# Kernel tuning notes

Measured on AMD Instinct MI355X. Metric: run time of the kernel, lower is better.

## Reference

```python
import jax, jax.numpy as jnp
import numpy as np

N, T = 64, 256
TOTAL_NODES, C_IN = 25, 128          # c = 3200
NUM_SEEDS, C_OUT = 5, 3              # seeds flat dim = 15
NEW_NODES = 20
LIN_IN = TOTAL_NODES * C_IN + NUM_SEEDS * C_OUT  # 3215


def setup_inputs() -> dict:
    key = jax.random.key(0)
    k1, k2, k3 = jax.random.split(key, 3)
    x = jax.random.normal(k1, (N, T, TOTAL_NODES * C_IN), dtype=jnp.float32)
    seeds = jax.random.normal(k2, (N, T, NUM_SEEDS, C_OUT), dtype=jnp.float32)
    # Stacked weights of the `new_nodes` cloned Linear(LIN_IN, C_OUT) layers.
    W = jax.random.normal(k3, (NEW_NODES, C_OUT, LIN_IN), dtype=jnp.float32) * 0.02
    b = jnp.zeros((NEW_NODES, C_OUT), dtype=jnp.float32)
    return {"x": x, "seeds": seeds, "W": W, "b": b}


def reference(x, seeds, W, b):
    n, t, _ = x.shape
    mix = jnp.concatenate([x, seeds.reshape(n, t, -1)], axis=2)  # [n,t,LIN_IN]
    # Fuse all cloned small Linears into one batched GEMM, then layout as
    # torch.stack([...], dim=3): output [n, t, c_out, new_nodes].
    out = jnp.einsum('ntc,koc->ntok', mix, W) + b.T  # b.T: [c_out, new_nodes]
    return out
```

## Files before the change

kernel.cpp:

```cpp
#include <hip/hip_runtime.h>


#define NROWS    16384
#define CIN      3200
#define SEED_K   15
#define LIN_IN   3215
#define NCOL     60
#define KB_MAIN  100
#define KB_TOT   101
#define WB_ELEMS (KB_TOT * 4 * 64 * 8)
#define PART_N   (NROWS * NCOL)

typedef __attribute__((ext_vector_type(8))) __bf16 bf16x8;
typedef __attribute__((ext_vector_type(4))) float f32x4;
typedef __attribute__((ext_vector_type(8))) unsigned short ushort8;

__device__ unsigned short Wb_g[WB_ELEMS];
__device__ __align__(16) float bias_g[64];

__device__ inline unsigned short f2bf_rne(float f) {
    unsigned int u = __builtin_bit_cast(unsigned int, f);
    u += 0x7fffu + ((u >> 16) & 1u);
    return (unsigned short)(u >> 16);
}

__device__ inline bf16x8 to_bf16x8(f32x4 a0, f32x4 a1) {
    ushort8 u;
    u[0] = f2bf_rne(a0[0]); u[1] = f2bf_rne(a0[1]);
    u[2] = f2bf_rne(a0[2]); u[3] = f2bf_rne(a0[3]);
    u[4] = f2bf_rne(a1[0]); u[5] = f2bf_rne(a1[1]);
    u[6] = f2bf_rne(a1[2]); u[7] = f2bf_rne(a1[3]);
    return __builtin_bit_cast(bf16x8, u);
}

__global__ void prep_B(const float* __restrict__ W, const float* __restrict__ b) {
    int idx = blockIdx.x * blockDim.x + threadIdx.x;
    if (idx >= WB_ELEMS) return;
    if (idx < 64) bias_g[idx] = (idx < NCOL) ? b[(idx % 20) * 3 + (idx / 20)] : 0.f;
    int jj   = idx & 7;
    int lane = (idx >> 3) & 63;
    int nt   = (idx >> 9) & 3;
    int kb   = idx >> 11;
    int k = kb * 32 + (lane >> 4) * 8 + jj;
    int n = nt * 16 + (lane & 15);
    float v = 0.0f;
    if (k < LIN_IN && n < NCOL) {
        int o = n / 20, kn = n % 20;
        v = W[(kn * 3 + o) * LIN_IN + k];
    }
    Wb_g[idx] = f2bf_rne(v);
}

__global__ __launch_bounds__(256, 6) void gen_nodes_part(
    const float* __restrict__ x, const float* __restrict__ seeds,
    float* __restrict__ part) {
    const int lane = threadIdx.x & 63;
    const int wave = threadIdx.x >> 6;
    const int quad = lane >> 4;
    const int l15  = lane & 15;
    const int rg   = blockIdx.x >> 1;
    const int kh   = blockIdx.x & 1;
    const int row_base = rg * 16;
    const int arow = row_base + l15;

    const float* xrow = x + (size_t)arow * CIN + quad * 8;

    f32x4 acc[4];
#pragma unroll
    for (int i = 0; i < 4; ++i) acc[i] = (f32x4){0.f, 0.f, 0.f, 0.f};

    const int kend = kh * 50 + 50;
    int kb = kh * 50 + wave;
    const f32x4* ap = (const f32x4*)(xrow + kb * 32);
    f32x4 a0 = __builtin_nontemporal_load(ap);
    f32x4 a1 = __builtin_nontemporal_load(ap + 1);

#pragma unroll 2
    while (kb < kend) {
        int kn = kb + 4;
        int kc = (kn < KB_MAIN - 1) ? kn : (KB_MAIN - 1);
        const f32x4* apn = (const f32x4*)(xrow + kc * 32);
        f32x4 p0 = __builtin_nontemporal_load(apn);
        f32x4 p1 = __builtin_nontemporal_load(apn + 1);

        const unsigned short* bb = Wb_g + (size_t)kb * 2048 + lane * 8;
        bf16x8 b0 = *(const bf16x8*)(bb);
        bf16x8 b1 = *(const bf16x8*)(bb + 512);
        bf16x8 b2 = *(const bf16x8*)(bb + 1024);
        bf16x8 b3 = *(const bf16x8*)(bb + 1536);
        bf16x8 af = to_bf16x8(a0, a1);
        acc[0] = __builtin_amdgcn_mfma_f32_16x16x32_bf16(af, b0, acc[0], 0, 0, 0);
        acc[1] = __builtin_amdgcn_mfma_f32_16x16x32_bf16(af, b1, acc[1], 0, 0, 0);
        acc[2] = __builtin_amdgcn_mfma_f32_16x16x32_bf16(af, b2, acc[2], 0, 0, 0);
        acc[3] = __builtin_amdgcn_mfma_f32_16x16x32_bf16(af, b3, acc[3], 0, 0, 0);

        a0 = p0; a1 = p1; kb = kn;
    }

    if (kh == 1 && wave == 3) {
        const float* srow = seeds + (size_t)arow * SEED_K;
        f32x4 s0 = {0.f, 0.f, 0.f, 0.f}, s1 = {0.f, 0.f, 0.f, 0.f};
#pragma unroll
        for (int j = 0; j < 4; ++j) {
            int c = quad * 8 + j;
            if (c < SEED_K) s0[j] = srow[c];
            if (c + 4 < SEED_K) s1[j] = srow[c + 4];
        }
        bf16x8 af = to_bf16x8(s0, s1);
        const unsigned short* bb = Wb_g + (size_t)KB_MAIN * 2048 + lane * 8;
        bf16x8 b0 = *(const bf16x8*)(bb);
        bf16x8 b1 = *(const bf16x8*)(bb + 512);
        bf16x8 b2 = *(const bf16x8*)(bb + 1024);
        bf16x8 b3 = *(const bf16x8*)(bb + 1536);
        acc[0] = __builtin_amdgcn_mfma_f32_16x16x32_bf16(af, b0, acc[0], 0, 0, 0);
        acc[1] = __builtin_amdgcn_mfma_f32_16x16x32_bf16(af, b1, acc[1], 0, 0, 0);
        acc[2] = __builtin_amdgcn_mfma_f32_16x16x32_bf16(af, b2, acc[2], 0, 0, 0);
        acc[3] = __builtin_amdgcn_mfma_f32_16x16x32_bf16(af, b3, acc[3], 0, 0, 0);
    }

    __shared__ float red[3][16][68];
    if (wave != 0) {
#pragma unroll
        for (int nt = 0; nt < 4; ++nt)
#pragma unroll
            for (int r = 0; r < 4; ++r)
                red[wave - 1][quad * 4 + r][nt * 16 + l15] = acc[nt][r];
    }
    __syncthreads();

    if (wave == 0) {
        float* pdst = part + (size_t)kh * PART_N;
#pragma unroll
        for (int nt = 0; nt < 4; ++nt) {
            int j = nt * 16 + l15;
            if (j < NCOL) {
#pragma unroll
                for (int r = 0; r < 4; ++r) {
                    int m = quad * 4 + r;
                    float v = acc[nt][r] + red[0][m][j] + red[1][m][j] + red[2][m][j];
                    pdst[(size_t)(row_base + m) * NCOL + j] = v;
                }
            }
        }
    }
}

__global__ __launch_bounds__(256) void combine(
    const float* __restrict__ part, float* __restrict__ out) {
    int idx = blockIdx.x * 256 + threadIdx.x;
    int fl  = idx * 4;
    f32x4 p0 = *(const f32x4*)(part + fl);
    f32x4 p1 = *(const f32x4*)(part + PART_N + fl);
    int jb = fl % NCOL;
    f32x4 bv = *(const f32x4*)(bias_g + jb);
    f32x4 o = p0 + p1 + bv;
    *(f32x4*)(out + fl) = o;
}

extern "C" void kernel_launch(void* const* d_in, const int* in_sizes, int n_in,
                              void* d_out, int out_size, void* d_ws, size_t ws_size,
                              hipStream_t stream) {
    const float* x     = (const float*)d_in[0];
    const float* seeds = (const float*)d_in[1];
    const float* W     = (const float*)d_in[2];
    const float* b     = (const float*)d_in[3];
    float* out  = (float*)d_out;
    float* part = (float*)d_ws;

    prep_B<<<(WB_ELEMS + 255) / 256, 256, 0, stream>>>(W, b);
    gen_nodes_part<<<2048, 256, 0, stream>>>(x, seeds, part);
    combine<<<PART_N / 4 / 256, 256, 0, stream>>>(part, out);
}
```

Baseline: 310.6 us.

## Process two 16-row tiles per block to reuse each B fragment load

Each block now handles 32 rows instead of 16, issuing two A-tile loads per k-step and reusing the same four bf16 B fragments for eight MFMAs. The grid is halved, occupancy hint lowered to 4, and the shared reduction buffer doubled. This is meant to halve the weight reloads per row and give more memory-level parallelism per wave, at the cost of more registers and fewer resident blocks.

```diff
diff --git a/kernel.cpp b/kernel.cpp
--- a/kernel.cpp
+++ b/kernel.cpp
@@ -51,7 +51,7 @@
     Wb_g[idx] = f2bf_rne(v);
 }
 
-__global__ __launch_bounds__(256, 6) void gen_nodes_part(
+__global__ __launch_bounds__(256, 4) void gen_nodes_part(
     const float* __restrict__ x, const float* __restrict__ seeds,
     float* __restrict__ part) {
     const int lane = threadIdx.x & 63;
@@ -60,85 +60,109 @@
     const int l15  = lane & 15;
     const int rg   = blockIdx.x >> 1;
     const int kh   = blockIdx.x & 1;
-    const int row_base = rg * 16;
+    const int row_base = rg * 32;
     const int arow = row_base + l15;
 
-    const float* xrow = x + (size_t)arow * CIN + quad * 8;
+    const float* xrow0 = x + (size_t)arow * CIN + quad * 8;
+    const float* xrow1 = xrow0 + (size_t)16 * CIN;
 
-    f32x4 acc[4];
+    f32x4 acc[2][4];
 #pragma unroll
-    for (int i = 0; i < 4; ++i) acc[i] = (f32x4){0.f, 0.f, 0.f, 0.f};
+    for (int t = 0; t < 2; ++t)
+#pragma unroll
+        for (int i = 0; i < 4; ++i) acc[t][i] = (f32x4){0.f, 0.f, 0.f, 0.f};
 
     const int kend = kh * 50 + 50;
     int kb = kh * 50 + wave;
-    const f32x4* ap = (const f32x4*)(xrow + kb * 32);
-    f32x4 a0 = __builtin_nontemporal_load(ap);
-    f32x4 a1 = __builtin_nontemporal_load(ap + 1);
+    {
+        const f32x4* ap0 = (const f32x4*)(xrow0 + kb * 32);
+        const f32x4* ap1 = (const f32x4*)(xrow1 + kb * 32);
+        f32x4 a0 = __builtin_nontemporal_load(ap0);
+        f32x4 a1 = __builtin_nontemporal_load(ap0 + 1);
+        f32x4 a2 = __builtin_nontemporal_load(ap1);
+        f32x4 a3 = __builtin_nontemporal_load(ap1 + 1);
 
 #pragma unroll 2
-    while (kb < kend) {
-        int kn = kb + 4;
-        int kc = (kn < KB_MAIN - 1) ? kn : (KB_MAIN - 1);
-        const f32x4* apn = (const f32x4*)(xrow + kc * 32);
-        f32x4 p0 = __builtin_nontemporal_load(apn);
-        f32x4 p1 = __builtin_nontemporal_load(apn + 1);
+        while (kb < kend) {
+            int kn = kb + 4;
+            int kc = (kn < KB_MAIN - 1) ? kn : (KB_MAIN - 1);
+            const f32x4* apn0 = (const f32x4*)(xrow0 + kc * 32);
+            const f32x4* apn1 = (const f32x4*)(xrow1 + kc * 32);
+            f32x4 p0 = __builtin_nontemporal_load(apn0);
+            f32x4 p1 = __builtin_nontemporal_load(apn0 + 1);
+            f32x4 p2 = __builtin_nontemporal_load(apn1);
+            f32x4 p3 = __builtin_nontemporal_load(apn1 + 1);
 
-        const unsigned short* bb = Wb_g + (size_t)kb * 2048 + lane * 8;
-        bf16x8 b0 = *(const bf16x8*)(bb);
-        bf16x8 b1 = *(const bf16x8*)(bb + 512);
-        bf16x8 b2 = *(const bf16x8*)(bb + 1024);
-        bf16x8 b3 = *(const bf16x8*)(bb + 1536);
-        bf16x8 af = to_bf16x8(a0, a1);
-        acc[0] = __builtin_amdgcn_mfma_f32_16x16x32_bf16(af, b0, acc[0], 0, 0, 0);
-        acc[1] = __builtin_amdgcn_mfma_f32_16x16x32_bf16(af, b1, acc[1], 0, 0, 0);
-        acc[2] = __builtin_amdgcn_mfma_f32_16x16x32_bf16(af, b2, acc[2], 0, 0, 0);
-        acc[3] = __builtin_amdgcn_mfma_f32_16x16x32_bf16(af, b3, acc[3], 0, 0, 0);
+            const unsigned short* bb = Wb_g + (size_t)kb * 2048 + lane * 8;
+            bf16x8 b0 = *(const bf16x8*)(bb);
+            bf16x8 b1 = *(const bf16x8*)(bb + 512);
+            bf16x8 b2 = *(const bf16x8*)(bb + 1024);
+            bf16x8 b3 = *(const bf16x8*)(bb + 1536);
+            bf16x8 af0 = to_bf16x8(a0, a1);
+            bf16x8 af1 = to_bf16x8(a2, a3);
+            acc[0][0] = __builtin_amdgcn_mfma_f32_16x16x32_bf16(af0, b0, acc[0][0], 0, 0, 0);
+            acc[0][1] = __builtin_amdgcn_mfma_f32_16x16x32_bf16(af0, b1, acc[0][1], 0, 0, 0);
+            acc[0][2] = __builtin_amdgcn_mfma_f32_16x16x32_bf16(af0, b2, acc[0][2], 0, 0, 0);
+            acc[0][3] = __builtin_amdgcn_mfma_f32_16x16x32_bf16(af0, b3, acc[0][3], 0, 0, 0);
+            acc[1][0] = __builtin_amdgcn_mfma_f32_16x16x32_bf16(af1, b0, acc[1][0], 0, 0, 0);
+            acc[1][1] = __builtin_amdgcn_mfma_f32_16x16x32_bf16(af1, b1, acc[1][1], 0, 0, 0);
+            acc[1][2] = __builtin_amdgcn_mfma_f32_16x16x32_bf16(af1, b2, acc[1][2], 0, 0, 0);
+            acc[1][3] = __builtin_amdgcn_mfma_f32_16x16x32_bf16(af1, b3, acc[1][3], 0, 0, 0);
 
-        a0 = p0; a1 = p1; kb = kn;
+            a0 = p0; a1 = p1; a2 = p2; a3 = p3; kb = kn;
+        }
     }
 
     if (kh == 1 && wave == 3) {
-        const float* srow = seeds + (size_t)arow * SEED_K;
-        f32x4 s0 = {0.f, 0.f, 0.f, 0.f}, s1 = {0.f, 0.f, 0.f, 0.f};
-#pragma unroll
-        for (int j = 0; j < 4; ++j) {
-            int c = quad * 8 + j;
-            if (c < SEED_K) s0[j] = srow[c];
-            if (c + 4 < SEED_K) s1[j] = srow[c + 4];
-        }
-        bf16x8 af = to_bf16x8(s0, s1);
         const unsigned short* bb = Wb_g + (size_t)KB_MAIN * 2048 + lane * 8;
         bf16x8 b0 = *(const bf16x8*)(bb);
         bf16x8 b1 = *(const bf16x8*)(bb + 512);
         bf16x8 b2 = *(const bf16x8*)(bb + 1024);
         bf16x8 b3 = *(const bf16x8*)(bb + 1536);
-        acc[0] = __builtin_amdgcn_mfma_f32_16x16x32_bf16(af, b0, acc[0], 0, 0, 0);
-        acc[1] = __builtin_amdgcn_mfma_f32_16x16x32_bf16(af, b1, acc[1], 0, 0, 0);
-        acc[2] = __builtin_amdgcn_mfma_f32_16x16x32_bf16(af, b2, acc[2], 0, 0, 0);
-        acc[3] = __builtin_amdgcn_mfma_f32_16x16x32_bf16(af, b3, acc[3], 0, 0, 0);
+#pragma unroll
+        for (int t = 0; t < 2; ++t) {
+            const float* srow = seeds + (size_t)(arow + t * 16) * SEED_K;
+            f32x4 s0 = {0.f, 0.f, 0.f, 0.f}, s1 = {0.f, 0.f, 0.f, 0.f};
+#pragma unroll
+            for (int j = 0; j < 4; ++j) {
+                int c = quad * 8 + j;
+                if (c < SEED_K) s0[j] = srow[c];
+                if (c + 4 < SEED_K) s1[j] = srow[c + 4];
+            }
+            bf16x8 af = to_bf16x8(s0, s1);
+            acc[t][0] = __builtin_amdgcn_mfma_f32_16x16x32_bf16(af, b0, acc[t][0], 0, 0, 0);
+            acc[t][1] = __builtin_amdgcn_mfma_f32_16x16x32_bf16(af, b1, acc[t][1], 0, 0, 0);
+            acc[t][2] = __builtin_amdgcn_mfma_f32_16x16x32_bf16(af, b2, acc[t][2], 0, 0, 0);
+            acc[t][3] = __builtin_amdgcn_mfma_f32_16x16x32_bf16(af, b3, acc[t][3], 0, 0, 0);
+        }
     }
 
-    __shared__ float red[3][16][68];
+    __shared__ float red[3][32][68];
     if (wave != 0) {
 #pragma unroll
-        for (int nt = 0; nt < 4; ++nt)
+        for (int t = 0; t < 2; ++t)
 #pragma unroll
-            for (int r = 0; r < 4; ++r)
-                red[wave - 1][quad * 4 + r][nt * 16 + l15] = acc[nt][r];
+            for (int nt = 0; nt < 4; ++nt)
+#pragma unroll
+                for (int r = 0; r < 4; ++r)
+                    red[wave - 1][t * 16 + quad * 4 + r][nt * 16 + l15] = acc[t][nt][r];
     }
     __syncthreads();
 
     if (wave == 0) {
         float* pdst = part + (size_t)kh * PART_N;
 #pragma unroll
-        for (int nt = 0; nt < 4; ++nt) {
-            int j = nt * 16 + l15;
-            if (j < NCOL) {
+        for (int t = 0; t < 2; ++t) {
 #pragma unroll
-                for (int r = 0; r < 4; ++r) {
-                    int m = quad * 4 + r;
-                    float v = acc[nt][r] + red[0][m][j] + red[1][m][j] + red[2][m][j];
-                    pdst[(size_t)(row_base + m) * NCOL + j] = v;
+            for (int nt = 0; nt < 4; ++nt) {
+                int j = nt * 16 + l15;
+                if (j < NCOL) {
+#pragma unroll
+                    for (int r = 0; r < 4; ++r) {
+                        int m = t * 16 + quad * 4 + r;
+                        float v = acc[t][nt][r] + red[0][m][j] + red[1][m][j] + red[2][m][j];
+                        pdst[(size_t)(row_base + m) * NCOL + j] = v;
+                    }
                 }
             }
         }
@@ -168,6 +192,6 @@
     float* part = (float*)d_ws;
 
     prep_B<<<(WB_ELEMS + 255) / 256, 256, 0, stream>>>(W, b);
-    gen_nodes_part<<<2048, 256, 0, stream>>>(x, seeds, part);
+    gen_nodes_part<<<1024, 256, 0, stream>>>(x, seeds, part);
     combine<<<PART_N / 4 / 256, 256, 0, stream>>>(part, out);
 }
```

Result: no change. 307.8 us (-0.9%).
